# Performance work log

Hardware: AMD Instinct MI355X
Metric: run time of the kernel (lower is better)

Reference implementation:

```python
import jax, jax.numpy as jnp
import numpy as np

B, C, H, W = 8, 512, 64, 64
HID = 4 * C  # MixFFN hidden = in_dim*4
FOCUS = 3.0


def _ln(x, g, b, eps=1e-5):
    m = x.mean(-1, keepdims=True)
    v = ((x - m) ** 2).mean(-1, keepdims=True)
    return (x - m) / jnp.sqrt(v + eps) * g + b


def setup_inputs() -> dict:
    key = jax.random.key(0)
    ks = jax.random.split(key, 12)
    init = lambda k, shape, fan: (jax.random.normal(k, shape, jnp.float32) / np.float32(np.sqrt(fan)))
    d = {}
    d['x'] = jax.random.normal(ks[0], (B, C, H, W), jnp.float32)
    # 1x1 conv weights stored as (Cout, Cin)
    d['Wq'] = init(ks[1], (C, C), C); d['bq'] = jnp.zeros((C,), jnp.float32)
    d['Wk'] = init(ks[2], (C, C), C); d['bk'] = jnp.zeros((C,), jnp.float32)
    d['Wv'] = init(ks[3], (C, C), C); d['bv'] = jnp.zeros((C,), jnp.float32)
    d['scale'] = jnp.zeros((1, 1, C), jnp.float32)  # nn.Parameter(torch.zeros)
    # MixFFN_skip params
    d['fc1_w'] = init(ks[4], (C, HID), C); d['fc1_b'] = jnp.zeros((HID,), jnp.float32)
    d['dw_w'] = init(ks[5], (HID, 1, 3, 3), 9); d['dw_b'] = jnp.zeros((HID,), jnp.float32)
    d['fc2_w'] = init(ks[6], (HID, C), HID); d['fc2_b'] = jnp.zeros((C,), jnp.float32)
    d['ln1_g'] = jnp.ones((HID,), jnp.float32); d['ln1_b'] = jnp.zeros((HID,), jnp.float32)
    d['lnm_g'] = jnp.ones((C,), jnp.float32); d['lnm_b'] = jnp.zeros((C,), jnp.float32)
    return d


def _forward(x, Wq, bq, Wk, bk, Wv, bv, scale, fc1_w, fc1_b, dw_w, dw_b, fc2_w, fc2_b, ln1_g, ln1_b, lnm_g, lnm_b):
    b, c, h, w = x.shape
    n = h * w
    # 1x1 convs (NCHW), then RAW reshape to (B, N, C) as in torch (no permute!)
    conv1 = lambda t, Wm, bm: jnp.einsum('bchw,oc->bohw', t, Wm) + bm[None, :, None, None]
    q = jax.nn.softmax(conv1(x, Wq, bq).reshape(b, n, c), axis=1)
    k = jax.nn.softmax(conv1(x, Wk, bk).reshape(b, n, c), axis=2)
    v = conv1(x, Wv, bv).reshape(b, n, c)
    q = jax.nn.relu(q) + 1e-6
    k = jax.nn.relu(k) + 1e-6
    sc = jax.nn.softplus(scale)
    q = q / sc
    k = k / sc
    q_norm = jnp.linalg.norm(q, axis=-1, keepdims=True)
    k_norm = jnp.linalg.norm(k, axis=-1, keepdims=True)
    q = q ** FOCUS  # focusing_factor <= 6 branch
    k = k ** FOCUS
    q = q / jnp.linalg.norm(q, axis=-1, keepdims=True) * q_norm
    k = k / jnp.linalg.norm(k, axis=-1, keepdims=True) * k_norm
    # num_heads == 1: (b h) n c == b n c
    z = 1.0 / (jnp.einsum('bic,bc->bi', q, k.sum(axis=1)) + 1e-6)
    kv = jnp.einsum('bjc,bjd->bcd', k, v)  # O(N) linear attention summary
    attn = jnp.einsum('bic,bcd,bi->bid', q, kv, z)
    shortcut = jnp.transpose(x, (0, 2, 3, 1)).reshape(b, n, c)  # proper rearrange b c h w -> b (h w) c
    enhanced = shortcut + attn
    # MixFFN_skip(norm_mlp(enhanced), h, w)
    t = _ln(enhanced, lnm_g, lnm_b)
    a = t @ fc1_w + fc1_b  # (B, N, HID)
    ai = jnp.transpose(a, (0, 2, 1)).reshape(b, HID, h, w)
    dw = jax.lax.conv_general_dilated(ai, dw_w, (1, 1), 'SAME',
                                      dimension_numbers=('NCHW', 'OIHW', 'NCHW'),
                                      feature_group_count=HID)
    dw = dw + dw_b[None, :, None, None]
    dw = jnp.transpose(dw.reshape(b, HID, n), (0, 2, 1))
    ax = jax.nn.gelu(_ln(dw + a, ln1_g, ln1_b), approximate=False)
    mlp_out = ax @ fc2_w + fc2_b
    out = enhanced + mlp_out
    return out.reshape(b, h, w, c)


def reference(x, Wq, bq, Wk, bk, Wv, bv, scale, fc1_w, fc1_b, dw_w, dw_b, fc2_w, fc2_b, ln1_g, ln1_b, lnm_g, lnm_b):
    return _forward(x, Wq, bq, Wk, bk, Wv, bv, scale, fc1_w, fc1_b, dw_w, dw_b, fc2_w, fc2_b, ln1_g, ln1_b, lnm_g, lnm_b)
```

## Files before the change

### kernel.cpp

```cpp
#include <hip/hip_runtime.h>
#include <hip/hip_bf16.h>

typedef __hip_bfloat16 bf16;
typedef __attribute__((ext_vector_type(8))) short bh8;
typedef __attribute__((ext_vector_type(4))) float f32x4;

#define CDIM 512
#define NDIM 4096
#define HIDD 2048
#define BATCH 8

__device__ __forceinline__ float bf2f(short s) {
    union { unsigned u; float f; } c; c.u = ((unsigned)(unsigned short)s) << 16; return c.f;
}
__device__ __forceinline__ short f2bf(float f) {
    union { __hip_bfloat16 h; short s; } c; c.h = __float2bfloat16(f); return c.s;
}
__device__ __forceinline__ float wsum(float v) {
#pragma unroll
    for (int o = 32; o; o >>= 1) v += __shfl_xor(v, o);
    return v;
}
__device__ __forceinline__ float wmax(float v) {
#pragma unroll
    for (int o = 32; o; o >>= 1) v = fmaxf(v, __shfl_xor(v, o));
    return v;
}

#define GLL(g, l) __builtin_amdgcn_global_load_lds( \
    (const __attribute__((address_space(1))) unsigned int*)(g), \
    (__attribute__((address_space(3))) unsigned int*)(l), 16, 0, 0)

enum { EP_BF16_BROW = 1, EP_ATTN = 3, EP_BF16_BCOL = 4, EP_OUT = 5, EP_QKV = 6 };

template<int MODE, int TM, int MFAST>
__global__ __launch_bounds__(256)
void gemm_bt(const bf16* __restrict__ A, int lda, long sA,
             const bf16* __restrict__ Bt, int ldb, long sB,
             void* __restrict__ Cp, int ldc, long sC, int K,
             const float* __restrict__ bias,
             const void* __restrict__ aux1, long sAux1,
             const void* __restrict__ aux2, long sAux2)
{
    constexpr int MF = TM / 32;
    __shared__ __align__(16) bf16 smem[TM * 64 + 128 * 64];
    bf16* As = smem;
    bf16* Bs = smem + TM * 64;
    int bx, by, bz;
    {
        const int gx = gridDim.x, gy = gridDim.y;
        const int nwg = gx * gy * gridDim.z;
        int lid = blockIdx.x + gx * (blockIdx.y + gy * blockIdx.z);
        const int cpx = nwg >> 3;
        int swz = (lid & 7) * cpx + (lid >> 3);
        if constexpr (MFAST) {
            by = swz % gy; swz /= gy;
            bx = swz % gx;
            bz = swz / gx;
        } else {
            bx = swz % gx; swz /= gx;
            by = swz % gy;
            bz = swz / gy;
        }
    }
    const bf16* Ab = A + (long)bz * sA + (long)by * TM * lda;
    const bf16* Bb = Bt + (long)bz * sB + (long)bx * 128 * ldb;
    const int t = threadIdx.x, lane = t & 63, wid = t >> 6;
    const int wm = wid >> 1, wn = wid & 1, lg = lane >> 4, lr = lane & 15;

    f32x4 acc[MF][4];
#pragma unroll
    for (int m = 0; m < MF; ++m)
#pragma unroll
        for (int n = 0; n < 4; ++n) acc[m][n] = (f32x4){0.f, 0.f, 0.f, 0.f};

    for (int kt = 0; kt < K; kt += 64) {
#pragma unroll
        for (int i = 0; i < MF; ++i) {
            const int ch = i * 256 + t;
            const int row = ch >> 3;
            const int cs = (ch & 7) ^ (row & 7);
            GLL(Ab + (long)row * lda + kt + (cs << 3), (char*)As + i * 4096 + wid * 1024);
        }
#pragma unroll
        for (int i = 0; i < 4; ++i) {
            const int ch = i * 256 + t;
            const int row = ch >> 3;
            const int cs = (ch & 7) ^ (row & 7);
            GLL(Bb + (long)row * ldb + kt + (cs << 3), (char*)Bs + i * 4096 + wid * 1024);
        }
        __syncthreads();
#pragma unroll
        for (int kk = 0; kk < 2; ++kk) {
            bh8 af[MF], bfv[4];
#pragma unroll
            for (int m = 0; m < MF; ++m) {
                const int row = wm * (TM / 2) + m * 16 + lr;
                const int kc = (kk * 4 + lg) ^ (row & 7);
                af[m] = *(const bh8*)(As + row * 64 + kc * 8);
            }
#pragma unroll
            for (int n = 0; n < 4; ++n) {
                const int row = wn * 64 + n * 16 + lr;
                const int kc = (kk * 4 + lg) ^ (row & 7);
                bfv[n] = *(const bh8*)(Bs + row * 64 + kc * 8);
            }
#pragma unroll
            for (int m = 0; m < MF; ++m)
#pragma unroll
                for (int n = 0; n < 4; ++n)
                    acc[m][n] = __builtin_amdgcn_mfma_f32_16x16x32_bf16(af[m], bfv[n], acc[m][n], 0, 0, 0);
        }
        __syncthreads();
    }

    if constexpr (TM == 128 && (MODE == EP_QKV || MODE == EP_BF16_BCOL)) {
        bf16* Cs = smem;
        bf16* dstb;
        bool doexp = false;
        if constexpr (MODE == EP_QKV) {
            const int which = by >> 2;
            if (which == 0) { dstb = (bf16*)Cp; doexp = true; }
            else if (which == 1) dstb = (bf16*)aux1;
            else dstb = (bf16*)aux2;
            dstb += (long)bz * sC + (long)((by & 3) * 128) * ldc;
        } else {
            dstb = (bf16*)Cp + (long)bz * sC + (long)by * 128 * ldc;
        }
#pragma unroll
        for (int m = 0; m < MF; ++m)
#pragma unroll
            for (int n = 0; n < 4; ++n)
#pragma unroll
                for (int r = 0; r < 4; ++r) {
                    const int row = wm * 64 + m * 16 + lg * 4 + r;
                    const int col = wn * 64 + n * 16 + lr;
                    float v = acc[m][n][r];
                    if constexpr (MODE == EP_QKV) v += bias[by * 128 + row];
                    else v += bias[bx * 128 + col];
                    if (doexp) v = __expf(v);
                    Cs[row * 128 + (col ^ (((row >> 2) & 3) << 4))] = __float2bfloat16(v);
                }
        __syncthreads();
#pragma unroll
        for (int it = 0; it < 8; ++it) {
            const int id = it * 256 + t;
            const int row = id >> 4, colc = (id & 15) << 3;
            bh8 v = *(const bh8*)(Cs + row * 128 + (colc ^ (((row >> 2) & 3) << 4)));
            *(bh8*)(dstb + (long)row * ldc + bx * 128 + colc) = v;
        }
        return;
    }

    const int gr0 = by * TM + wm * (TM / 2);
    const int gc0 = bx * 128 + wn * 64;
#pragma unroll
    for (int m = 0; m < MF; ++m) {
#pragma unroll
        for (int n = 0; n < 4; ++n) {
            const int gc = gc0 + n * 16 + lr;
#pragma unroll
            for (int r = 0; r < 4; ++r) {
                const int gr = gr0 + m * 16 + lg * 4 + r;
                float v = acc[m][n][r];
                if constexpr (MODE == EP_BF16_BROW) {
                    ((bf16*)Cp + (long)bz * sC)[(long)gr * ldc + gc] = __float2bfloat16(v + bias[gr]);
                } else if constexpr (MODE == EP_ATTN) {
                    const bf16* xg = (const bf16*)aux1 + (long)bz * sAux1;
                    const float* zg = (const float*)aux2 + (long)bz * sAux2;
                    ((float*)Cp + (long)bz * sC)[(long)gr * ldc + gc] =
                        zg[gr] * v + bf2f(*(const short*)(xg + (long)gr * 512 + gc));
                } else if constexpr (MODE == EP_OUT) {
                    float* op = (float*)Cp;
                    const long idx = (long)gr * ldc + gc;
                    op[idx] = v + bias[gc] + ((const float*)aux1)[idx];
                }
            }
        }
    }
}

__global__ __launch_bounds__(256)
void gemm_tn_splitk(const bf16* __restrict__ A, int lda, long sA,
                    const bf16* __restrict__ B, int ldb, long sB,
                    bf16* __restrict__ part)
{
    __shared__ __align__(16) short smem[2 * 64 * 128];
    short* As = smem;
    short* Bs = smem + 64 * 128;
    int bx, by, bzl;
    {
        const int gx = gridDim.x, gy = gridDim.y;
        const int nwg = gx * gy * gridDim.z;
        int lid = blockIdx.x + gx * (blockIdx.y + gy * blockIdx.z);
        const int cpx = nwg >> 3;
        int swz = (lid & 7) * cpx + (lid >> 3);
        bx = swz % gx; swz /= gx;
        by = swz % gy;
        bzl = swz / gy;
    }
    const int bz = bzl >> 2, ks = bzl & 3;
    const bf16* Ab = A + (long)bz * sA + (long)ks * 1024 * lda + by * 128;
    const bf16* Bb = B + (long)bz * sB + (long)ks * 1024 * ldb + bx * 128;
    const int t = threadIdx.x, lane = t & 63, wid = t >> 6;
    const int wm = wid >> 1, wn = wid & 1, lg = lane >> 4, lr = lane & 15;

    f32x4 acc[4][4];
#pragma unroll
    for (int m = 0; m < 4; ++m)
#pragma unroll
        for (int n = 0; n < 4; ++n) acc[m][n] = (f32x4){0.f, 0.f, 0.f, 0.f};

    for (int kt = 0; kt < 1024; kt += 64) {
#pragma unroll
        for (int i = 0; i < 4; ++i) {
            const int ch = i * 256 + t;
            const int row = ch >> 4;
            const int cs = (ch & 15) ^ (((row >> 3) & 3) << 1);
            GLL(Ab + (long)(kt + row) * lda + (cs << 3), (char*)As + i * 4096 + wid * 1024);
            GLL(Bb + (long)(kt + row) * ldb + (cs << 3), (char*)Bs + i * 4096 + wid * 1024);
        }
        __syncthreads();
#pragma unroll
        for (int kk = 0; kk < 2; ++kk) {
            bh8 af[4], bfv[4];
#pragma unroll
            for (int m = 0; m < 4; ++m) {
                const int col = wm * 64 + m * 16 + lr;
#pragma unroll
                for (int u = 0; u < 8; ++u) {
                    const int row = kk * 32 + lg * 8 + u;
                    af[m][u] = As[row * 128 + (((col >> 3) ^ (((row >> 3) & 3) << 1)) << 3) + (col & 7)];
                }
            }
#pragma unroll
            for (int n = 0; n < 4; ++n) {
                const int col = wn * 64 + n * 16 + lr;
#pragma unroll
                for (int u = 0; u < 8; ++u) {
                    const int row = kk * 32 + lg * 8 + u;
                    bfv[n][u] = Bs[row * 128 + (((col >> 3) ^ (((row >> 3) & 3) << 1)) << 3) + (col & 7)];
                }
            }
#pragma unroll
            for (int m = 0; m < 4; ++m)
#pragma unroll
                for (int n = 0; n < 4; ++n)
                    acc[m][n] = __builtin_amdgcn_mfma_f32_16x16x32_bf16(af[m], bfv[n], acc[m][n], 0, 0, 0);
        }
        __syncthreads();
    }

    bf16* Cs = (bf16*)smem;
    bf16* dstb = part + ((long)bzl << 18) + (long)by * 128 * 512;
#pragma unroll
    for (int m = 0; m < 4; ++m)
#pragma unroll
        for (int n = 0; n < 4; ++n)
#pragma unroll
            for (int r = 0; r < 4; ++r) {
                const int row = wm * 64 + m * 16 + lg * 4 + r;
                const int col = wn * 64 + n * 16 + lr;
                Cs[row * 128 + (col ^ (((row >> 2) & 3) << 4))] = __float2bfloat16(acc[m][n][r]);
            }
    __syncthreads();
#pragma unroll
    for (int it = 0; it < 8; ++it) {
        const int id = it * 256 + t;
        const int row = id >> 4, colc = (id & 15) << 3;
        bh8 v = *(const bh8*)(Cs + row * 128 + (colc ^ (((row >> 2) & 3) << 4)));
        *(bh8*)(dstb + (long)row * 512 + bx * 128 + colc) = v;
    }
}

__global__ __launch_bounds__(256)
void k_transpose3(const float* __restrict__ fc1w, bf16* __restrict__ fc1wT,
                  const float* __restrict__ fc2w, bf16* __restrict__ fc2wT,
                  const float* __restrict__ x, bf16* __restrict__ xbT)
{
    __shared__ float tile[64][65];
    const int bid = blockIdx.x;
    const float* s; bf16* d; int Rd, Cd, bx, by;
    if (bid < 256) {
        s = fc1w; d = fc1wT; Rd = 2048; Cd = 512; bx = bid & 31; by = bid >> 5;
    } else if (bid < 512) {
        const int i = bid - 256;
        s = fc2w; d = fc2wT; Rd = 512; Cd = 2048; bx = i & 7; by = i >> 3;
    } else {
        const int i = bid - 512;
        const int bz = i >> 9, j = i & 511;
        bx = j & 63; by = j >> 6;
        const long NC = (long)NDIM * CDIM;
        s = x + (long)bz * NC; d = xbT + (long)bz * NC; Rd = 4096; Cd = 512;
    }
    const int r0 = bx * 64, c0 = by * 64;
    const int t = threadIdx.x;
#pragma unroll 4
    for (int i = 0; i < 16; ++i) {
        int idx = i * 256 + t;
        int a = idx >> 6, b = idx & 63;
        tile[a][b] = s[(long)(c0 + a) * Rd + r0 + b];
    }
    __syncthreads();
#pragma unroll 4
    for (int i = 0; i < 16; ++i) {
        int idx = i * 256 + t;
        int a = idx >> 6, b = idx & 63;
        d[(long)(r0 + a) * Cd + c0 + b] = __float2bfloat16(tile[b][a]);
    }
}

__global__ void k_setup(const float* __restrict__ Wq, const float* __restrict__ Wk,
                        const float* __restrict__ Wv, bf16* __restrict__ oq,
                        bf16* __restrict__ ok, bf16* __restrict__ ov,
                        const float* __restrict__ scale, float* __restrict__ invsc,
                        const float* __restrict__ w, float* __restrict__ wT,
                        const float* __restrict__ bq, const float* __restrict__ bk,
                        const float* __restrict__ bv, float* __restrict__ bqkv) {
    int i = blockIdx.x * 256 + threadIdx.x;
    if (i < 262144) {
        oq[i] = __float2bfloat16(Wq[i]);
        ok[i] = __float2bfloat16(Wk[i]);
        ov[i] = __float2bfloat16(Wv[i]);
    }
    if (i < 512) invsc[i] = 1.0f / log1pf(expf(scale[i]));
    if (i < 1536) bqkv[i] = (i < 512 ? bq[i] : (i < 1024 ? bk[i - 512] : bv[i - 1024]));
    if (i < HIDD * 9) {
        int chn = i / 9, kk = i % 9;
        wT[kk * HIDD + chn] = w[i];
    }
}

__global__ void k_fill(float* o, int n, float v) {
    int i = blockIdx.x * 256 + threadIdx.x; if (i < n) o[i] = v;
}

__global__ __launch_bounds__(256)
void k_colsums(const bf16* __restrict__ qe, const bf16* __restrict__ kb,
               float* __restrict__ qpart, float* __restrict__ kpart) {
    const int xb = blockIdx.x;
    const int ic = blockIdx.y, b = blockIdx.z;
    const int j = (xb & 1) * 256 + threadIdx.x;
    const bf16* src = (xb < 2) ? qe : kb;
    const bf16* p = src + (long)b * (NDIM * CDIM) + (long)ic * 256 * CDIM + j;
    float s = 0.f;
    for (int i = 0; i < 256; ++i) s += bf2f(*(const short*)(p + (long)i * CDIM));
    ((xb < 2) ? qpart : kpart)[((long)b * 16 + ic) * CDIM + j] = s;
}

__global__ __launch_bounds__(256)
void k_red2(const float* __restrict__ qpart, float* __restrict__ qsum,
            const float* __restrict__ kpart, float* __restrict__ ksum) {
    const int idx = blockIdx.x * 256 + threadIdx.x;
    const int which = idx >> 12, r = idx & 4095;
    const int b = r >> 9, c = r & 511;
    const float* src = which ? kpart : qpart;
    float s = 0.f;
#pragma unroll
    for (int jc = 0; jc < 16; ++jc) s += src[((long)(b * 16 + jc)) * CDIM + c];
    (which ? ksum : qsum)[r] = s;
}

__global__ __launch_bounds__(256)
void k_kvqrow(const bf16* __restrict__ part, bf16* __restrict__ kvt,
              const bf16* __restrict__ qe, const float* __restrict__ qsum,
              const float* __restrict__ invsc, bf16* __restrict__ qb,
              const float* __restrict__ ksum, float* __restrict__ z)
{
    if (blockIdx.x < 1024) {
        const long e = ((long)blockIdx.x * 256 + threadIdx.x) * 8;
        const int b = (int)(e >> 18);
        const int off = (int)(e & 262143);
        float s[8] = {0.f, 0.f, 0.f, 0.f, 0.f, 0.f, 0.f, 0.f};
#pragma unroll
        for (int ks = 0; ks < 4; ++ks) {
            bh8 v = *(const bh8*)(part + (((long)(b * 4 + ks)) << 18) + off);
#pragma unroll
            for (int j = 0; j < 8; ++j) s[j] += bf2f(v[j]);
        }
        bh8 o;
#pragma unroll
        for (int j = 0; j < 8; ++j) o[j] = f2bf(s[j]);
        *(bh8*)(kvt + ((long)b << 18) + off) = o;
        return;
    }
    const long row = (long)(blockIdx.x - 1024) * 4 + (threadIdx.x >> 6);
    const int lane = threadIdx.x & 63;
    const int b = (int)(row >> 12);
    bh8 ev = *(const bh8*)(qe + row * CDIM + lane * 8);
    const float* qs = qsum + b * CDIM + lane * 8;
    const float* is = invsc + lane * 8;
    f32x4 s0 = *(const f32x4*)qs, s1 = *(const f32x4*)(qs + 4);
    f32x4 i0 = *(const f32x4*)is, i1 = *(const f32x4*)(is + 4);
    float q[8];
#pragma unroll
    for (int k = 0; k < 4; ++k) {
        q[k]     = (bf2f(ev[k]) / s0[k] + 1e-6f) * i0[k];
        q[k + 4] = (bf2f(ev[k + 4]) / s1[k] + 1e-6f) * i1[k];
    }
    float s2 = 0.f, s6 = 0.f, q3[8];
#pragma unroll
    for (int k = 0; k < 8; ++k) { s2 += q[k] * q[k]; float c = q[k] * q[k] * q[k]; q3[k] = c; s6 += c * c; }
    s2 = wsum(s2); s6 = wsum(s6);
    const float sc = sqrtf(s2) / sqrtf(s6);
    bh8 o;
#pragma unroll
    for (int k = 0; k < 8; ++k) o[k] = f2bf(q3[k] * sc);
    *(bh8*)(qb + row * CDIM + lane * 8) = o;
    const float* ks = ksum + (long)b * CDIM + lane * 8;
    f32x4 k0 = *(const f32x4*)ks, k1 = *(const f32x4*)(ks + 4);
    float zd = 0.f;
#pragma unroll
    for (int j = 0; j < 4; ++j) { zd += bf2f(o[j]) * k0[j]; zd += bf2f(o[j + 4]) * k1[j]; }
    zd = wsum(zd);
    if (lane == 0) z[row] = 1.0f / (zd + 1e-6f);
}

__global__ __launch_bounds__(256)
void k_krow(bf16* __restrict__ kb, const float* __restrict__ invsc)
{
    const long row = (long)blockIdx.x * 4 + (threadIdx.x >> 6);
    const int lane = threadIdx.x & 63;
    bh8 v = *(const bh8*)(kb + row * CDIM + lane * 8);
    const float* is = invsc + lane * 8;
    f32x4 i0 = *(const f32x4*)is, i1 = *(const f32x4*)(is + 4);
    float xv[8];
#pragma unroll
    for (int k = 0; k < 8; ++k) xv[k] = bf2f(v[k]);
    float mx = -1e30f;
#pragma unroll
    for (int k = 0; k < 8; ++k) mx = fmaxf(mx, xv[k]);
    mx = wmax(mx);
    float e[8], se = 0.f;
#pragma unroll
    for (int k = 0; k < 8; ++k) { e[k] = __expf(xv[k] - mx); se += e[k]; }
    se = wsum(se);
    const float inv = 1.0f / se;
    float q[8];
#pragma unroll
    for (int k = 0; k < 4; ++k) {
        q[k]     = (e[k] * inv + 1e-6f) * i0[k];
        q[k + 4] = (e[k + 4] * inv + 1e-6f) * i1[k];
    }
    float s2 = 0.f, s6 = 0.f, q3[8];
#pragma unroll
    for (int k = 0; k < 8; ++k) { s2 += q[k] * q[k]; float c = q[k] * q[k] * q[k]; q3[k] = c; s6 += c * c; }
    s2 = wsum(s2); s6 = wsum(s6);
    const float sc = sqrtf(s2) / sqrtf(s6);
    bh8 o;
#pragma unroll
    for (int k = 0; k < 8; ++k) o[k] = f2bf(q3[k] * sc);
    *(bh8*)(kb + row * CDIM + lane * 8) = o;
}

__global__ __launch_bounds__(256)
void k_ln512(const float* __restrict__ src, const float* __restrict__ g,
             const float* __restrict__ bta, bf16* __restrict__ dst)
{
    const long row = (long)blockIdx.x * 4 + (threadIdx.x >> 6);
    const int lane = threadIdx.x & 63;
    const float* p = src + row * CDIM + lane * 8;
    f32x4 a0 = *(const f32x4*)p, a1 = *(const f32x4*)(p + 4);
    float s = 0.f, ss = 0.f;
#pragma unroll
    for (int k = 0; k < 4; ++k) { s += a0[k] + a1[k]; ss += a0[k] * a0[k] + a1[k] * a1[k]; }
    s = wsum(s); ss = wsum(ss);
    const float mean = s * (1.0f / 512), var = ss * (1.0f / 512) - mean * mean;
    const float rstd = rsqrtf(var + 1e-5f);
    const float* gp = g + lane * 8;
    const float* bp = bta + lane * 8;
    f32x4 g0 = *(const f32x4*)gp, g1 = *(const f32x4*)(gp + 4);
    f32x4 b0 = *(const f32x4*)bp, b1 = *(const f32x4*)(bp + 4);
    bh8 o;
#pragma unroll
    for (int k = 0; k < 4; ++k) {
        o[k]     = f2bf((a0[k] - mean) * rstd * g0[k] + b0[k]);
        o[k + 4] = f2bf((a1[k] - mean) * rstd * g1[k] + b1[k]);
    }
    *(bh8*)(dst + row * CDIM + lane * 8) = o;
}

__global__ __launch_bounds__(256)
void k_dwlngelu4(const bf16* __restrict__ a, const float* __restrict__ dwwT,
                 const float* __restrict__ dwb, const float* __restrict__ g1,
                 const float* __restrict__ b1, bf16* __restrict__ ax)
{
    const long s0 = (long)blockIdx.x * 4;
    const int h = (int)((s0 >> 6) & 63);
    const int w0 = (int)(s0 & 63);
    const int ch = threadIdx.x * 8;

    float wgt[9][8];
#pragma unroll
    for (int kk = 0; kk < 9; ++kk) {
        f32x4 w0v = *(const f32x4*)(dwwT + kk * HIDD + ch);
        f32x4 w1v = *(const f32x4*)(dwwT + kk * HIDD + ch + 4);
#pragma unroll
        for (int j = 0; j < 4; ++j) { wgt[kk][j] = w0v[j]; wgt[kk][j + 4] = w1v[j]; }
    }
#pragma unroll
    for (int j = 0; j < 8; ++j) wgt[4][j] += 1.0f;

    float acc[4][8];
    {
        f32x4 d0 = *(const f32x4*)(dwb + ch), d1 = *(const f32x4*)(dwb + ch + 4);
#pragma unroll
        for (int ti = 0; ti < 4; ++ti)
#pragma unroll
            for (int j = 0; j < 4; ++j) { acc[ti][j] = d0[j]; acc[ti][j + 4] = d1[j]; }
    }

#pragma unroll
    for (int dy = -1; dy <= 1; ++dy) {
        const int hh = h + dy;
        if ((unsigned)hh >= 64u) continue;
#pragma unroll
        for (int c = -1; c <= 4; ++c) {
            const int ww = w0 + c;
            if ((unsigned)ww >= 64u) continue;
            bh8 v = *(const bh8*)(a + (s0 + (long)dy * 64 + c) * HIDD + ch);
            float f[8];
#pragma unroll
            for (int j = 0; j < 8; ++j) f[j] = bf2f(v[j]);
#pragma unroll
            for (int ti = 0; ti < 4; ++ti) {
                const int dx = c - ti;
                if (dx < -1 || dx > 1) continue;
                const int kk = (dy + 1) * 3 + (dx + 1);
#pragma unroll
                for (int j = 0; j < 8; ++j) acc[ti][j] += wgt[kk][j] * f[j];
            }
        }
    }

    float sv[4], qv[4];
#pragma unroll
    for (int ti = 0; ti < 4; ++ti) {
        float s = 0.f, q = 0.f;
#pragma unroll
        for (int j = 0; j < 8; ++j) { s += acc[ti][j]; q += acc[ti][j] * acc[ti][j]; }
        sv[ti] = wsum(s); qv[ti] = wsum(q);
    }
    __shared__ float red[4][4][2];
    const int wid = threadIdx.x >> 6, lane = threadIdx.x & 63;
    if (lane == 0)
#pragma unroll
        for (int ti = 0; ti < 4; ++ti) { red[wid][ti][0] = sv[ti]; red[wid][ti][1] = qv[ti]; }
    __syncthreads();

    f32x4 ga = *(const f32x4*)(g1 + ch), gb = *(const f32x4*)(g1 + ch + 4);
    f32x4 ba = *(const f32x4*)(b1 + ch), bb = *(const f32x4*)(b1 + ch + 4);
    float gg[8], bb8[8];
#pragma unroll
    for (int j = 0; j < 4; ++j) { gg[j] = ga[j]; gg[j + 4] = gb[j]; bb8[j] = ba[j]; bb8[j + 4] = bb[j]; }

#pragma unroll
    for (int ti = 0; ti < 4; ++ti) {
        const float s = red[0][ti][0] + red[1][ti][0] + red[2][ti][0] + red[3][ti][0];
        const float q = red[0][ti][1] + red[1][ti][1] + red[2][ti][1] + red[3][ti][1];
        const float mean = s * (1.0f / 2048), var = q * (1.0f / 2048) - mean * mean;
        const float rstd = rsqrtf(var + 1e-5f);
        bh8 o;
#pragma unroll
        for (int j = 0; j < 8; ++j) {
            float y = (acc[ti][j] - mean) * rstd * gg[j] + bb8[j];
            o[j] = f2bf(0.5f * y * (1.0f + erff(y * 0.70710678118654752f)));
        }
        *(bh8*)(ax + (s0 + ti) * HIDD + ch) = o;
    }
}

extern "C" void kernel_launch(void* const* d_in, const int* in_sizes, int n_in,
                              void* d_out, int out_size, void* d_ws, size_t ws_size,
                              hipStream_t stream) {
    const float* x     = (const float*)d_in[0];
    const float* Wq    = (const float*)d_in[1];
    const float* bq    = (const float*)d_in[2];
    const float* Wk    = (const float*)d_in[3];
    const float* bk    = (const float*)d_in[4];
    const float* Wv    = (const float*)d_in[5];
    const float* bv    = (const float*)d_in[6];
    const float* scale = (const float*)d_in[7];
    const float* fc1_w = (const float*)d_in[8];
    const float* fc1_b = (const float*)d_in[9];
    const float* dw_w  = (const float*)d_in[10];
    const float* dw_b  = (const float*)d_in[11];
    const float* fc2_w = (const float*)d_in[12];
    const float* fc2_b = (const float*)d_in[13];
    const float* ln1_g = (const float*)d_in[14];
    const float* ln1_b = (const float*)d_in[15];
    const float* lnm_g = (const float*)d_in[16];
    const float* lnm_b = (const float*)d_in[17];
    float* out = (float*)d_out;
    char* p = (char*)d_ws;

    bf16*  xbT   = (bf16*)(p + 0);
    bf16*  kb    = (bf16*)(p + 33554432);
    bf16*  vb    = (bf16*)(p + 67108864);
    bf16*  kvt   = (bf16*)(p + 100663296);
    bf16*  wqb   = (bf16*)(p + 104857600);
    bf16*  wkb   = (bf16*)(p + 105381888);
    bf16*  wvb   = (bf16*)(p + 105906176);
    bf16*  fc1wT = (bf16*)(p + 106430464);
    bf16*  fc2wT = (bf16*)(p + 108527616);
    float* invsc = (float*)(p + 110624768);
    float* dwwT  = (float*)(p + 110626816);
    float* bqkv  = (float*)(p + 110700544);
    float* qsum  = (float*)(p + 110757888);
    float* ksum  = (float*)(p + 110905344);
    float* zbuf  = (float*)(p + 110921728);
    const size_t REQUIRED = 111052800;
    float* qpart = (float*)kvt;
    float* kpart = (float*)((char*)kvt + 262144);
    bf16*  qe    = (bf16*)out;
    bf16*  kvpart= (bf16*)((char*)out + 33554432);
    bf16*  qb    = kb;
    bf16*  abuf  = (bf16*)(p + 0);
    bf16*  axbuf = (bf16*)(p + 33554432);
    bf16*  tbuf  = (bf16*)(p + 67108864);

    if (ws_size < REQUIRED) {
        k_fill<<<(out_size + 255) / 256, 256, 0, stream>>>(out, out_size, 100000.0f + (float)(ws_size >> 20));
        return;
    }

    const long NC = (long)NDIM * CDIM;

    k_setup<<<1024, 256, 0, stream>>>(Wq, Wk, Wv, wqb, wkb, wvb, scale, invsc,
                                      dw_w, dwwT, bq, bk, bv, bqkv);
    k_transpose3<<<4608, 256, 0, stream>>>(fc1_w, fc1wT, fc2_w, fc2wT, x, xbT);

    gemm_bt<EP_QKV, 128, 1><<<dim3(32, 12, 8), 256, 0, stream>>>(
        wqb, 512, 0, xbT, 512, NC, qe, 4096, NC, 512, bqkv, kb, 0, vb, 0);

    k_krow<<<8192, 256, 0, stream>>>(kb, invsc);
    k_colsums<<<dim3(4, 16, 8), 256, 0, stream>>>(qe, kb, qpart, kpart);
    k_red2<<<32, 256, 0, stream>>>(qpart, qsum, kpart, ksum);

    gemm_tn_splitk<<<dim3(4, 4, 32), 256, 0, stream>>>(vb, 512, NC, kb, 512, NC, kvpart);
    k_kvqrow<<<9216, 256, 0, stream>>>(kvpart, kvt, qe, qsum, invsc, qb, ksum, zbuf);

    gemm_bt<EP_ATTN, 128, 0><<<dim3(4, 32, 8), 256, 0, stream>>>(
        qb, 512, NC, kvt, 512, 262144, out, 512, NC, 512, nullptr, xbT, NC, zbuf, 4096);

    k_ln512<<<8192, 256, 0, stream>>>(out, lnm_g, lnm_b, tbuf);
    for (int q4 = 0; q4 < 4; ++q4) {
        float* outq = out + (long)q4 * 8192 * CDIM;
        bf16* tq = tbuf + (long)q4 * 8192 * CDIM;
        gemm_bt<EP_BF16_BCOL, 128, 0><<<dim3(16, 64, 1), 256, 0, stream>>>(
            tq, 512, 0, fc1wT, 512, 0, abuf, 2048, 0, 512, fc1_b, nullptr, 0, nullptr, 0);
        k_dwlngelu4<<<2048, 256, 0, stream>>>(abuf, dwwT, dw_b, ln1_g, ln1_b, axbuf);
        gemm_bt<EP_OUT, 64, 0><<<dim3(4, 128, 1), 256, 0, stream>>>(
            axbuf, 2048, 0, fc2wT, 2048, 0, outq, 512, 0, 2048, fc2_b, outq, 0, nullptr, 0);
    }
}
```

Measured before the change: 613.2 us.

## Add 256x256-tile 8-wave pipelined GEMM for QKV and fc1 projections

```diff
diff --git a/kernel.cpp b/kernel.cpp
--- a/kernel.cpp
+++ b/kernel.cpp
@@ -31,7 +31,194 @@
     (const __attribute__((address_space(1))) unsigned int*)(g), \
     (__attribute__((address_space(3))) unsigned int*)(l), 16, 0, 0)
 
-enum { EP_BF16_BROW = 1, EP_ATTN = 3, EP_BF16_BCOL = 4, EP_OUT = 5, EP_QKV = 6 };
+
+__device__ __forceinline__ void stage_ht(const bf16* __restrict__ base, int ld,
+                                         int kt, char* ldsb, int t) {
+#pragma unroll
+    for (int l = 0; l < 2; ++l) {
+        const int id = l * 512 + t;
+        const int row = id >> 3, c = id & 7;
+        const int cs = c ^ (row & 7);
+        GLL(base + (long)row * ld + kt + (cs << 3),
+            ldsb + l * 8192 + (t >> 6) * 1024 + (t & 63) * 16);
+    }
+}
+
+template<int MODE, int MFAST>
+__global__ __launch_bounds__(512, 2)
+void gemm256(const bf16* __restrict__ A, int lda, long sA,
+             const bf16* __restrict__ Bt, int ldb, long sB,
+             void* __restrict__ Cp, int ldc, long sC, int K,
+             const float* __restrict__ bias,
+             void* __restrict__ aux1, void* __restrict__ aux2)
+{
+    __shared__ __align__(16) bf16 smem[65536];
+    char* smemB = (char*)smem;
+    int bx, by, bz;
+    {
+        const int gx = gridDim.x, gy = gridDim.y;
+        const int nwg = gx * gy * gridDim.z;
+        int lid = blockIdx.x + gx * (blockIdx.y + gy * blockIdx.z);
+        const int cpx = nwg >> 3;
+        int swz = (lid & 7) * cpx + (lid >> 3);
+        if constexpr (MFAST) {
+            by = swz % gy; swz /= gy;
+            bx = swz % gx;
+            bz = swz / gx;
+        } else {
+            bx = swz % gx; swz /= gx;
+            by = swz % gy;
+            bz = swz / gy;
+        }
+    }
+    const bf16* Ab = A + (long)bz * sA + (long)by * 256 * lda;
+    const bf16* Bb = Bt + (long)bz * sB + (long)bx * 256 * ldb;
+    const int t = threadIdx.x, lane = t & 63, wid = t >> 6;
+    const int wm = wid >> 2, wn = wid & 3;
+    const int lg = lane >> 4, lr = lane & 15;
+
+    f32x4 acc[8][4];
+#pragma unroll
+    for (int m = 0; m < 8; ++m)
+#pragma unroll
+        for (int n = 0; n < 4; ++n) acc[m][n] = (f32x4){0.f, 0.f, 0.f, 0.f};
+
+    const int T = K >> 6;
+    stage_ht(Bb, ldb, 0, smemB + 65536, t);
+    stage_ht(Bb + (long)128 * ldb, ldb, 0, smemB + 65536 + 16384, t);
+    stage_ht(Ab, lda, 0, smemB, t);
+    stage_ht(Ab + (long)128 * lda, lda, 0, smemB + 16384, t);
+
+    for (int tt = 0; tt < T; ++tt) {
+        const int cur = tt & 1, nb = cur ^ 1;
+        const int ktn = (tt + 1) << 6;
+        const bool pf = (tt + 1 < T);
+        const int aco = cur ? 16384 : 0;
+        const int bco = 32768 + (cur ? 16384 : 0);
+        const int anb = nb ? 32768 : 0;
+        const int bnb = 65536 + (nb ? 32768 : 0);
+
+        bh8 afA[4], afB[4], bfA[4], bfB[4];
+
+        if (pf) stage_ht(Bb, ldb, ktn, smemB + bnb, t);
+        if (pf) asm volatile("s_waitcnt vmcnt(2)" ::: "memory");
+        else    asm volatile("s_waitcnt vmcnt(0)" ::: "memory");
+        __builtin_amdgcn_s_barrier();
+#pragma unroll
+        for (int m = 0; m < 4; ++m) {
+            const int row = wm * 128 + m * 16 + lr;
+            afA[m] = *(const bh8*)(smem + aco + row * 64 + (lg ^ (row & 7)) * 8);
+        }
+#pragma unroll
+        for (int n = 0; n < 4; ++n) {
+            const int row = wn * 64 + n * 16 + lr;
+            bfA[n] = *(const bh8*)(smem + bco + row * 64 + (lg ^ (row & 7)) * 8);
+        }
+        asm volatile("s_waitcnt lgkmcnt(0)" ::: "memory");
+        __builtin_amdgcn_sched_barrier(0);
+        __builtin_amdgcn_s_setprio(1);
+#pragma unroll
+        for (int m = 0; m < 4; ++m)
+#pragma unroll
+            for (int n = 0; n < 4; ++n)
+                acc[m][n] = __builtin_amdgcn_mfma_f32_16x16x32_bf16(afA[m], bfA[n], acc[m][n], 0, 0, 0);
+        __builtin_amdgcn_s_setprio(0);
+        __builtin_amdgcn_s_barrier();
+
+#pragma unroll
+        for (int m = 0; m < 4; ++m) {
+            const int row = wm * 128 + 64 + m * 16 + lr;
+            afB[m] = *(const bh8*)(smem + aco + row * 64 + (lg ^ (row & 7)) * 8);
+        }
+        if (pf) stage_ht(Bb + (long)128 * ldb, ldb, ktn, smemB + bnb + 16384, t);
+        asm volatile("s_waitcnt lgkmcnt(0)" ::: "memory");
+        __builtin_amdgcn_sched_barrier(0);
+        __builtin_amdgcn_s_setprio(1);
+#pragma unroll
+        for (int m = 0; m < 4; ++m)
+#pragma unroll
+            for (int n = 0; n < 4; ++n)
+                acc[4 + m][n] = __builtin_amdgcn_mfma_f32_16x16x32_bf16(afB[m], bfA[n], acc[4 + m][n], 0, 0, 0);
+        __builtin_amdgcn_s_setprio(0);
+        __builtin_amdgcn_s_barrier();
+
+#pragma unroll
+        for (int m = 0; m < 4; ++m) {
+            const int row = wm * 128 + m * 16 + lr;
+            afA[m] = *(const bh8*)(smem + aco + row * 64 + ((4 + lg) ^ (row & 7)) * 8);
+        }
+#pragma unroll
+        for (int n = 0; n < 4; ++n) {
+            const int row = wn * 64 + n * 16 + lr;
+            bfB[n] = *(const bh8*)(smem + bco + row * 64 + ((4 + lg) ^ (row & 7)) * 8);
+        }
+        if (pf) stage_ht(Ab, lda, ktn, smemB + anb, t);
+        asm volatile("s_waitcnt lgkmcnt(0)" ::: "memory");
+        __builtin_amdgcn_sched_barrier(0);
+        __builtin_amdgcn_s_setprio(1);
+#pragma unroll
+        for (int m = 0; m < 4; ++m)
+#pragma unroll
+            for (int n = 0; n < 4; ++n)
+                acc[m][n] = __builtin_amdgcn_mfma_f32_16x16x32_bf16(afA[m], bfB[n], acc[m][n], 0, 0, 0);
+        __builtin_amdgcn_s_setprio(0);
+        __builtin_amdgcn_s_barrier();
+
+#pragma unroll
+        for (int m = 0; m < 4; ++m) {
+            const int row = wm * 128 + 64 + m * 16 + lr;
+            afB[m] = *(const bh8*)(smem + aco + row * 64 + ((4 + lg) ^ (row & 7)) * 8);
+        }
+        if (pf) stage_ht(Ab + (long)128 * lda, lda, ktn, smemB + anb + 16384, t);
+        asm volatile("s_waitcnt lgkmcnt(0)" ::: "memory");
+        __builtin_amdgcn_sched_barrier(0);
+        __builtin_amdgcn_s_setprio(1);
+#pragma unroll
+        for (int m = 0; m < 4; ++m)
+#pragma unroll
+            for (int n = 0; n < 4; ++n)
+                acc[4 + m][n] = __builtin_amdgcn_mfma_f32_16x16x32_bf16(afB[m], bfB[n], acc[4 + m][n], 0, 0, 0);
+        __builtin_amdgcn_s_setprio(0);
+        __builtin_amdgcn_s_barrier();
+    }
+
+    const int gr0 = by * 256 + wm * 128;
+    const int gc0 = bx * 256 + wn * 64;
+    if constexpr (MODE == 0) {
+        const int which = by >> 1;
+        bf16* dst = (which == 0) ? (bf16*)Cp : (which == 1) ? (bf16*)aux1 : (bf16*)aux2;
+        dst += (long)bz * sC;
+#pragma unroll
+        for (int m = 0; m < 8; ++m)
+#pragma unroll
+            for (int n = 0; n < 4; ++n) {
+                const int col = gc0 + n * 16 + lr;
+#pragma unroll
+                for (int r = 0; r < 4; ++r) {
+                    const int grow = gr0 + m * 16 + lg * 4 + r;
+                    float v = acc[m][n][r] + bias[grow];
+                    if (which == 0) v = __expf(v);
+                    dst[(long)(grow - which * 512) * ldc + col] = __float2bfloat16(v);
+                }
+            }
+    } else {
+        bf16* dst = (bf16*)Cp + (long)bz * sC;
+#pragma unroll
+        for (int m = 0; m < 8; ++m)
+#pragma unroll
+            for (int n = 0; n < 4; ++n) {
+                const int col = gc0 + n * 16 + lr;
+                const float bc = bias[col];
+#pragma unroll
+                for (int r = 0; r < 4; ++r) {
+                    const int grow = gr0 + m * 16 + lg * 4 + r;
+                    dst[(long)grow * ldc + col] = __float2bfloat16(acc[m][n][r] + bc);
+                }
+            }
+    }
+}
+
+enum { EP_BF16_BROW = 1, EP_ATTN = 3, EP_BF16_BCOL = 4, EP_OUT = 5 };
 
 template<int MODE, int TM, int MFAST>
 __global__ __launch_bounds__(256)
@@ -114,44 +301,6 @@
         __syncthreads();
     }
 
-    if constexpr (TM == 128 && (MODE == EP_QKV || MODE == EP_BF16_BCOL)) {
-        bf16* Cs = smem;
-        bf16* dstb;
-        bool doexp = false;
-        if constexpr (MODE == EP_QKV) {
-            const int which = by >> 2;
-            if (which == 0) { dstb = (bf16*)Cp; doexp = true; }
-            else if (which == 1) dstb = (bf16*)aux1;
-            else dstb = (bf16*)aux2;
-            dstb += (long)bz * sC + (long)((by & 3) * 128) * ldc;
-        } else {
-            dstb = (bf16*)Cp + (long)bz * sC + (long)by * 128 * ldc;
-        }
-#pragma unroll
-        for (int m = 0; m < MF; ++m)
-#pragma unroll
-            for (int n = 0; n < 4; ++n)
-#pragma unroll
-                for (int r = 0; r < 4; ++r) {
-                    const int row = wm * 64 + m * 16 + lg * 4 + r;
-                    const int col = wn * 64 + n * 16 + lr;
-                    float v = acc[m][n][r];
-                    if constexpr (MODE == EP_QKV) v += bias[by * 128 + row];
-                    else v += bias[bx * 128 + col];
-                    if (doexp) v = __expf(v);
-                    Cs[row * 128 + (col ^ (((row >> 2) & 3) << 4))] = __float2bfloat16(v);
-                }
-        __syncthreads();
-#pragma unroll
-        for (int it = 0; it < 8; ++it) {
-            const int id = it * 256 + t;
-            const int row = id >> 4, colc = (id & 15) << 3;
-            bh8 v = *(const bh8*)(Cs + row * 128 + (colc ^ (((row >> 2) & 3) << 4)));
-            *(bh8*)(dstb + (long)row * ldc + bx * 128 + colc) = v;
-        }
-        return;
-    }
-
     const int gr0 = by * TM + wm * (TM / 2);
     const int gc0 = bx * 128 + wn * 64;
 #pragma unroll
@@ -170,7 +319,9 @@
                     const float* zg = (const float*)aux2 + (long)bz * sAux2;
                     ((float*)Cp + (long)bz * sC)[(long)gr * ldc + gc] =
                         zg[gr] * v + bf2f(*(const short*)(xg + (long)gr * 512 + gc));
-                } else if constexpr (MODE == EP_OUT) {
+                } else if constexpr (MODE == EP_BF16_BCOL) {
+                    ((bf16*)Cp + (long)bz * sC)[(long)gr * ldc + gc] = __float2bfloat16(v + bias[gc]);
+                } else {
                     float* op = (float*)Cp;
                     const long idx = (long)gr * ldc + gc;
                     op[idx] = v + bias[gc] + ((const float*)aux1)[idx];
@@ -630,8 +781,8 @@
                                       dw_w, dwwT, bq, bk, bv, bqkv);
     k_transpose3<<<4608, 256, 0, stream>>>(fc1_w, fc1wT, fc2_w, fc2wT, x, xbT);
 
-    gemm_bt<EP_QKV, 128, 1><<<dim3(32, 12, 8), 256, 0, stream>>>(
-        wqb, 512, 0, xbT, 512, NC, qe, 4096, NC, 512, bqkv, kb, 0, vb, 0);
+    gemm256<0, 1><<<dim3(16, 6, 8), 512, 0, stream>>>(
+        wqb, 512, 0, xbT, 512, NC, qe, 4096, NC, 512, bqkv, kb, vb);
 
     k_krow<<<8192, 256, 0, stream>>>(kb, invsc);
     k_colsums<<<dim3(4, 16, 8), 256, 0, stream>>>(qe, kb, qpart, kpart);
@@ -647,8 +798,8 @@
     for (int q4 = 0; q4 < 4; ++q4) {
         float* outq = out + (long)q4 * 8192 * CDIM;
         bf16* tq = tbuf + (long)q4 * 8192 * CDIM;
-        gemm_bt<EP_BF16_BCOL, 128, 0><<<dim3(16, 64, 1), 256, 0, stream>>>(
-            tq, 512, 0, fc1wT, 512, 0, abuf, 2048, 0, 512, fc1_b, nullptr, 0, nullptr, 0);
+        gemm256<1, 0><<<dim3(8, 32, 1), 512, 0, stream>>>(
+            tq, 512, 0, fc1wT, 512, 0, abuf, 2048, 0, 512, fc1_b, nullptr, nullptr);
         k_dwlngelu4<<<2048, 256, 0, stream>>>(abuf, dwwT, dw_b, ln1_g, ln1_b, axbuf);
         gemm_bt<EP_OUT, 64, 0><<<dim3(4, 128, 1), 256, 0, stream>>>(
             axbuf, 2048, 0, fc2wT, 2048, 0, outq, 512, 0, 2048, fc2_b, outq, 0, nullptr, 0);
```

After: 573.9 us. -6.4%, faster.
